# Kernel optimization log

Measured on AMD Instinct MI355X. Metric: run time of the kernel, lower is better.

## Reference

```python
import jax, jax.numpy as jnp
import numpy as np

IN_FEATURES = 128
OUT_FEATURES = 128


def setup_inputs() -> dict:
    key = jax.random.key(0)
    k1, k2, k3 = jax.random.split(key, 3)
    h_i = jax.random.normal(k1, (IN_FEATURES,), dtype=jnp.float32)
    h_j = jax.random.normal(k2, (200000, OUT_FEATURES), dtype=jnp.float32)
    a = jax.random.normal(k3, (IN_FEATURES + OUT_FEATURES, 1), dtype=jnp.float32)
    return {"h_i": h_i, "h_j": h_j, "a": a}


def reference(h_i, h_j, a):
    # e_n = dot(concat(h_i, h_j[n]), a) = h_i . a[:in] + h_j[n] . a[in:]
    a_i = a[:IN_FEATURES, 0]   # [in]
    a_j = a[IN_FEATURES:, 0]   # [out]
    logits = jnp.dot(h_i, a_i) + h_j @ a_j        # [N]
    attention = jax.nn.softmax(logits, axis=0)    # [N]
    # dropout is identity in eval mode (training=False)
    h_prime = attention @ h_j                     # [out]
    return jax.nn.elu(h_prime)                    # concat=True -> ELU
```

## Files before the change

kernel.cpp:

```cpp
#include <hip/hip_runtime.h>
#include <hip/hip_bf16.h>
#include <math.h>

#define COLS 128

__global__ __launch_bounds__(256, 4) void gat_pass1(
    const float* __restrict__ hj, const float* __restrict__ a,
    float* __restrict__ pacc, float* __restrict__ pm, float* __restrict__ pl,
    int nrows, int nblocks) {
  const int w    = threadIdx.x >> 6;
  const int lane = threadIdx.x & 63;
  const int gw   = blockIdx.x * 4 + w;
  const int total_w = nblocks * 4;

  const float aj0 = a[COLS + 2 * lane];
  const float aj1 = a[COLS + 2 * lane + 1];

  float m = -INFINITY, l = 0.f, acc0 = 0.f, acc1 = 0.f;

  for (int r = gw; r < nrows; r += total_w) {
    const float2 v = ((const float2*)(hj + (size_t)r * COLS))[lane];
    float p = v.x * aj0 + v.y * aj1;
    #pragma unroll
    for (int off = 1; off < 64; off <<= 1) p += __shfl_xor(p, off, 64);
    const float mn    = fmaxf(m, p);
    const float alpha = __expf(m - mn);
    const float wgt   = __expf(p - mn);
    l    = l * alpha + wgt;
    acc0 = acc0 * alpha + wgt * v.x;
    acc1 = acc1 * alpha + wgt * v.y;
    m = mn;
  }

  __shared__ float sm[4], sl[4], sacc[4][COLS];
  sacc[w][2 * lane]     = acc0;
  sacc[w][2 * lane + 1] = acc1;
  if (lane == 0) { sm[w] = m; sl[w] = l; }
  __syncthreads();

  const int t = threadIdx.x;
  const float Mb = fmaxf(fmaxf(sm[0], sm[1]), fmaxf(sm[2], sm[3]));
  if (t < COLS) {
    float s = 0.f;
    #pragma unroll
    for (int ww = 0; ww < 4; ww++) s += __expf(sm[ww] - Mb) * sacc[ww][t];
    pacc[(size_t)blockIdx.x * COLS + t] = s;
  }
  if (t == 0) {
    float lb = 0.f;
    #pragma unroll
    for (int ww = 0; ww < 4; ww++) lb += __expf(sm[ww] - Mb) * sl[ww];
    pm[blockIdx.x] = Mb;
    pl[blockIdx.x] = lb;
  }
}

__global__ __launch_bounds__(256) void gat_pass2(
    const float* __restrict__ pacc, const float* __restrict__ pm,
    const float* __restrict__ pl, float* __restrict__ out, int nblocks) {
  const int col = blockIdx.x;
  const int t   = threadIdx.x;
  __shared__ float sM[4], sz[4], sc[4];

  float local = -INFINITY;
  for (int b = t; b < nblocks; b += 256) local = fmaxf(local, pm[b]);
  #pragma unroll
  for (int off = 1; off < 64; off <<= 1) local = fmaxf(local, __shfl_xor(local, off, 64));
  if ((t & 63) == 0) sM[t >> 6] = local;
  __syncthreads();
  const float M = fmaxf(fmaxf(sM[0], sM[1]), fmaxf(sM[2], sM[3]));

  float zs = 0.f, cs = 0.f;
  for (int b = t; b < nblocks; b += 256) {
    const float e = __expf(pm[b] - M);
    zs += e * pl[b];
    cs += e * pacc[(size_t)b * COLS + col];
  }
  #pragma unroll
  for (int off = 1; off < 64; off <<= 1) {
    zs += __shfl_xor(zs, off, 64);
    cs += __shfl_xor(cs, off, 64);
  }
  if ((t & 63) == 0) { sz[t >> 6] = zs; sc[t >> 6] = cs; }
  __syncthreads();

  if (t == 0) {
    const float Z = sz[0] + sz[1] + sz[2] + sz[3];
    const float C = sc[0] + sc[1] + sc[2] + sc[3];
    const float h = C / Z;
    out[col] = h > 0.f ? h : expm1f(h);
  }
}

extern "C" void kernel_launch(void* const* d_in, const int* in_sizes, int n_in,
                              void* d_out, int out_size, void* d_ws, size_t ws_size,
                              hipStream_t stream) {
  const float* hj = (const float*)d_in[1];
  const float* a  = (const float*)d_in[2];
  float* out = (float*)d_out;

  const int nrows = in_sizes[1] / COLS;

  const size_t per_block = (COLS + 2) * sizeof(float);
  int nblocks = 1024;
  if (ws_size < (size_t)nblocks * per_block) {
    nblocks = (int)(ws_size / per_block);
    if (nblocks > 256) nblocks &= ~63;
    if (nblocks < 1) nblocks = 1;
  }
  float* pacc = (float*)d_ws;
  float* pm   = pacc + (size_t)nblocks * COLS;
  float* pl   = pm + nblocks;

  gat_pass1<<<nblocks, 256, 0, stream>>>(hj, a, pacc, pm, pl, nrows, nblocks);
  gat_pass2<<<COLS, 256, 0, stream>>>(pacc, pm, pl, out, nblocks);
}
```

Baseline: 165.7 us.

## Process two rows per wavefront with float4 loads and branchy online softmax

Each wavefront is split into two 32-lane halves, and each half handles one row using float4 loads, so the cross-lane reduction uses 5 shuffle steps instead of 6. The row loop is unrolled by two and the online softmax update branches so that only one exponential is computed per row. The grid grows to 2048 blocks of 8 units each, and the block combine computes the per-unit scale factors once. The branch can diverge between the two halves, and the partial-result count feeding pass 2 doubles.

```diff
diff --git a/kernel.cpp b/kernel.cpp
--- a/kernel.cpp
+++ b/kernel.cpp
@@ -1,56 +1,103 @@
 #include <hip/hip_runtime.h>
-#include <hip/hip_bf16.h>
 #include <math.h>
 
 #define COLS 128
 
-__global__ __launch_bounds__(256, 4) void gat_pass1(
+__global__ __launch_bounds__(256) void gat_pass1(
     const float* __restrict__ hj, const float* __restrict__ a,
     float* __restrict__ pacc, float* __restrict__ pm, float* __restrict__ pl,
-    int nrows, int nblocks) {
-  const int w    = threadIdx.x >> 6;
-  const int lane = threadIdx.x & 63;
-  const int gw   = blockIdx.x * 4 + w;
-  const int total_w = nblocks * 4;
+    int nrows, int nunits) {
+  const int t    = threadIdx.x;
+  const int wave = t >> 6;
+  const int lane = t & 63;
+  const int half = lane >> 5;
+  const int sub  = lane & 31;
+  const int uib  = wave * 2 + half;
+  const int unit = blockIdx.x * 8 + uib;
 
-  const float aj0 = a[COLS + 2 * lane];
-  const float aj1 = a[COLS + 2 * lane + 1];
+  const float4 aj = ((const float4*)(a + COLS))[sub];
 
-  float m = -INFINITY, l = 0.f, acc0 = 0.f, acc1 = 0.f;
+  float m = -INFINITY, l = 0.f;
+  float ax = 0.f, ay = 0.f, az = 0.f, aw = 0.f;
 
-  for (int r = gw; r < nrows; r += total_w) {
-    const float2 v = ((const float2*)(hj + (size_t)r * COLS))[lane];
-    float p = v.x * aj0 + v.y * aj1;
+  const int stride = nunits;
+  int r = unit;
+
+  for (; r + stride < nrows; r += 2 * stride) {
+    const float4 v0 = ((const float4*)(hj + (size_t)r * COLS))[sub];
+    const float4 v1 = ((const float4*)(hj + (size_t)(r + stride) * COLS))[sub];
+
+    float p0 = v0.x * aj.x + v0.y * aj.y + v0.z * aj.z + v0.w * aj.w;
     #pragma unroll
-    for (int off = 1; off < 64; off <<= 1) p += __shfl_xor(p, off, 64);
-    const float mn    = fmaxf(m, p);
-    const float alpha = __expf(m - mn);
-    const float wgt   = __expf(p - mn);
-    l    = l * alpha + wgt;
-    acc0 = acc0 * alpha + wgt * v.x;
-    acc1 = acc1 * alpha + wgt * v.y;
-    m = mn;
+    for (int off = 1; off <= 16; off <<= 1) p0 += __shfl_xor(p0, off, 64);
+    if (p0 <= m) {
+      const float w = __expf(p0 - m);
+      l += w; ax += w * v0.x; ay += w * v0.y; az += w * v0.z; aw += w * v0.w;
+    } else {
+      const float alpha = __expf(m - p0);
+      l = l * alpha + 1.f;
+      ax = ax * alpha + v0.x; ay = ay * alpha + v0.y;
+      az = az * alpha + v0.z; aw = aw * alpha + v0.w;
+      m = p0;
+    }
+
+    float p1 = v1.x * aj.x + v1.y * aj.y + v1.z * aj.z + v1.w * aj.w;
+    #pragma unroll
+    for (int off = 1; off <= 16; off <<= 1) p1 += __shfl_xor(p1, off, 64);
+    if (p1 <= m) {
+      const float w = __expf(p1 - m);
+      l += w; ax += w * v1.x; ay += w * v1.y; az += w * v1.z; aw += w * v1.w;
+    } else {
+      const float alpha = __expf(m - p1);
+      l = l * alpha + 1.f;
+      ax = ax * alpha + v1.x; ay = ay * alpha + v1.y;
+      az = az * alpha + v1.z; aw = aw * alpha + v1.w;
+      m = p1;
+    }
+  }
+  for (; r < nrows; r += stride) {
+    const float4 v0 = ((const float4*)(hj + (size_t)r * COLS))[sub];
+    float p0 = v0.x * aj.x + v0.y * aj.y + v0.z * aj.z + v0.w * aj.w;
+    #pragma unroll
+    for (int off = 1; off <= 16; off <<= 1) p0 += __shfl_xor(p0, off, 64);
+    if (p0 <= m) {
+      const float w = __expf(p0 - m);
+      l += w; ax += w * v0.x; ay += w * v0.y; az += w * v0.z; aw += w * v0.w;
+    } else {
+      const float alpha = __expf(m - p0);
+      l = l * alpha + 1.f;
+      ax = ax * alpha + v0.x; ay = ay * alpha + v0.y;
+      az = az * alpha + v0.z; aw = aw * alpha + v0.w;
+      m = p0;
+    }
   }
 
-  __shared__ float sm[4], sl[4], sacc[4][COLS];
-  sacc[w][2 * lane]     = acc0;
-  sacc[w][2 * lane + 1] = acc1;
-  if (lane == 0) { sm[w] = m; sl[w] = l; }
+  __shared__ float sm[8], sl[8], se[8], sMb;
+  __shared__ float sacc[8][COLS];
+  ((float4*)sacc[uib])[sub] = make_float4(ax, ay, az, aw);
+  if (sub == 0) { sm[uib] = m; sl[uib] = l; }
   __syncthreads();
 
-  const int t = threadIdx.x;
-  const float Mb = fmaxf(fmaxf(sm[0], sm[1]), fmaxf(sm[2], sm[3]));
+  if (t < 8) {
+    float Mb = sm[0];
+    #pragma unroll
+    for (int u = 1; u < 8; u++) Mb = fmaxf(Mb, sm[u]);
+    se[t] = __expf(sm[t] - Mb);
+    if (t == 0) sMb = Mb;
+  }
+  __syncthreads();
+
   if (t < COLS) {
     float s = 0.f;
     #pragma unroll
-    for (int ww = 0; ww < 4; ww++) s += __expf(sm[ww] - Mb) * sacc[ww][t];
+    for (int u = 0; u < 8; u++) s += se[u] * sacc[u][t];
     pacc[(size_t)blockIdx.x * COLS + t] = s;
   }
   if (t == 0) {
     float lb = 0.f;
     #pragma unroll
-    for (int ww = 0; ww < 4; ww++) lb += __expf(sm[ww] - Mb) * sl[ww];
-    pm[blockIdx.x] = Mb;
+    for (int u = 0; u < 8; u++) lb += se[u] * sl[u];
+    pm[blockIdx.x] = sMb;
     pl[blockIdx.x] = lb;
   }
 }
@@ -101,17 +148,19 @@
 
   const int nrows = in_sizes[1] / COLS;
 
+  int nblocks = 2048;
   const size_t per_block = (COLS + 2) * sizeof(float);
-  int nblocks = 1024;
   if (ws_size < (size_t)nblocks * per_block) {
     nblocks = (int)(ws_size / per_block);
-    if (nblocks > 256) nblocks &= ~63;
+    if (nblocks > 64) nblocks &= ~63;
     if (nblocks < 1) nblocks = 1;
   }
+  const int nunits = nblocks * 8;
+
   float* pacc = (float*)d_ws;
   float* pm   = pacc + (size_t)nblocks * COLS;
   float* pl   = pm + nblocks;
 
-  gat_pass1<<<nblocks, 256, 0, stream>>>(hj, a, pacc, pm, pl, nrows, nblocks);
+  gat_pass1<<<nblocks, 256, 0, stream>>>(hj, a, pacc, pm, pl, nrows, nunits);
   gat_pass2<<<COLS, 256, 0, stream>>>(pacc, pm, pl, out, nblocks);
 }
```

After: 155.9 us. 5.9% less time.
